# Kernel tuning notes

Measured on AMD Instinct MI355X. Metric: run time of the kernel, lower is better.

## Reference

```python
import jax, jax.numpy as jnp
import numpy as np

DIM = 512
HEADS = 8
RES = 14
HEAD_DIM = DIM // HEADS
N = RES * RES


def _make_bias_idxs(res):
    pts = [(i, j) for i in range(res) for j in range(res)]
    offs = {}
    idxs = []
    for p1 in pts:
        for p2 in pts:
            o = (abs(p1[0] - p2[0]), abs(p1[1] - p2[1]))
            if o not in offs:
                offs[o] = len(offs)
            idxs.append(offs[o])
    return np.asarray(idxs, dtype=np.int32).reshape(res * res, res * res), len(offs)


def setup_inputs() -> dict:
    key = jax.random.key(0)
    ks = jax.random.split(key, 6)
    idxs, n_off = _make_bias_idxs(RES)  # n_off == 196 for res=14
    B = 128
    return {
        "x": jax.random.normal(ks[0], (B, DIM, RES, RES), dtype=jnp.float32),
        "qkv_w": jax.random.normal(ks[1], (3 * DIM, DIM), dtype=jnp.float32) * 0.02,
        "qkv_b": jnp.zeros((3 * DIM,), dtype=jnp.float32),
        "proj_w": jax.random.normal(ks[2], (DIM, DIM), dtype=jnp.float32) * 0.02,
        "proj_b": jnp.zeros((DIM,), dtype=jnp.float32),
        "attention_biases": jax.random.normal(ks[3], (HEADS, n_off), dtype=jnp.float32) * 0.02,
        "bias_idxs": jnp.asarray(idxs),
    }


def reference(x, qkv_w, qkv_b, proj_w, proj_b, attention_biases, bias_idxs):
    B, C, H, W = x.shape
    scale = HEAD_DIM ** -0.5
    # 1x1 conv == channel-wise linear
    qkv = jnp.einsum("oc,bchw->bohw", qkv_w, x) + qkv_b[None, :, None, None]
    q, k, v = jnp.split(qkv, 3, axis=1)
    # [B, heads, head_dim, N]
    q = q.reshape(B, HEADS, HEAD_DIM, N)
    k = k.reshape(B, HEADS, HEAD_DIM, N)
    v = v.reshape(B, HEADS, HEAD_DIM, N)
    attn = jnp.einsum("bhdn,bhdm->bhnm", q, k) * scale  # [B,h,N,N]
    bias = attention_biases[:, bias_idxs]  # gather -> [h,N,N]
    attn = jax.nn.softmax(attn + bias[None], axis=-1)
    out = jnp.einsum("bhnm,bhdm->bhdn", attn, v).reshape(B, C, H, W)
    return jnp.einsum("oc,bchw->bohw", proj_w, out) + proj_b[None, :, None, None]
```

## Files before the change

### kernel.cpp

```cpp
#include <hip/hip_runtime.h>
#include <hip/hip_bf16.h>
#include <math.h>

#define B_     128
#define DIM_   512
#define HEADS_ 8
#define HD_    64
#define N_     196
#define NP_    224
#define NROW_  208
#define SCALE_ 0.125f
#define BSTRIDE (DIM_ * N_)
#define J_     (B_ * NP_)

typedef unsigned short u16;
typedef unsigned int   u32;
typedef __attribute__((ext_vector_type(8))) short bf16x8;
typedef __attribute__((ext_vector_type(4))) float f32x4;

__device__ __forceinline__ u16 f2bf(float f) {
    u32 u = __float_as_uint(f);
    return (u16)((u + 0x7fffu + ((u >> 16) & 1u)) >> 16);
}
__device__ __forceinline__ void gload_lds16(const u16* g, u16* l) {
    __builtin_amdgcn_global_load_lds(
        (const __attribute__((address_space(1))) void*)g,
        (__attribute__((address_space(3))) void*)l, 16, 0, 0);
}

__global__ __launch_bounds__(256) void cvt_bf(
    const float* __restrict__ src, u16* __restrict__ dst, int n4)
{
    const int i = blockIdx.x * 256 + threadIdx.x;
    if (i < n4) {
        const float4 v = reinterpret_cast<const float4*>(src)[i];
        uint2 o;
        o.x = (u32)f2bf(v.x) | ((u32)f2bf(v.y) << 16);
        o.y = (u32)f2bf(v.z) | ((u32)f2bf(v.w) << 16);
        reinterpret_cast<uint2*>(dst)[i] = o;
    }
}

__global__ __launch_bounds__(256) void cvt_xT(
    const float* __restrict__ x, u16* __restrict__ XT)
{
    __shared__ float tile[64][65];
    const int t = threadIdx.x;
    const int jj = t & 63, ii = t >> 6;
    const int ct = blockIdx.x, ntb = blockIdx.y, b = blockIdx.z;
    const float* xb = x + ((size_t)b * DIM_ + ct * 64) * N_;
    const int n0 = ntb * 64;
    #pragma unroll
    for (int s = 0; s < 16; ++s) {
        const int i = ii + s * 4;
        const int n = n0 + jj;
        tile[i][jj] = (n < N_) ? xb[(size_t)i * N_ + n] : 0.f;
    }
    __syncthreads();
    u16* ot = XT + (size_t)b * NP_ * DIM_ + ct * 64;
    #pragma unroll
    for (int s = 0; s < 16; ++s) {
        const int nn = n0 + ii + s * 4;
        if (nn < N_) ot[(size_t)nn * DIM_ + jj] = f2bf(tile[jj][ii + s * 4]);
    }
}

__global__ __launch_bounds__(256) void mk_eb(
    const float* __restrict__ biases, const int* __restrict__ bidx,
    float* __restrict__ EB)
{
    const int n = blockIdx.x, h = blockIdx.y;
    const int m = threadIdx.x;
    if (m < NP_) {
        float v = 0.f;
        if (n < N_ && m < N_) v = __expf(biases[h * N_ + bidx[n * N_ + m]]);
        EB[((size_t)h * NROW_ + n) * NP_ + m] = v;
    }
}

template<bool QKV>
__global__ __launch_bounds__(256) void gemm128(
    const u16* __restrict__ Bt, const u16* __restrict__ W,
    const float* __restrict__ bias,
    u16* __restrict__ o_q, u16* __restrict__ o_k, u16* __restrict__ o_v,
    float* __restrict__ o_f)
{
    __shared__ u16 As[128 * 32];
    __shared__ u16 Bs[128 * 32];
    const int t = threadIdx.x;
    const int wave = t >> 6, lane = t & 63;
    const int m16 = lane & 15, quad = lane >> 4;
    const int jt = blockIdx.x, mt = blockIdx.y;
    const int m0 = mt * 128, j0 = jt * 128;
    const int wy = wave >> 1, wx = wave & 1;

    const int srow  = (lane >> 2);
    const int schnk = (lane & 3) ^ ((lane >> 3) & 3);
    const u16* gA = W  + (size_t)(m0 + wave * 32 + srow) * DIM_ + schnk * 8;
    const u16* gB = Bt + (size_t)(j0 + wave * 32 + srow) * DIM_ + schnk * 8;

    const int rcol = (quad ^ ((m16 >> 1) & 3)) * 8;

    f32x4 acc[4][4];
    const f32x4 z4 = {0.f, 0.f, 0.f, 0.f};
    #pragma unroll
    for (int fi = 0; fi < 4; ++fi)
        #pragma unroll
        for (int fj = 0; fj < 4; ++fj) acc[fi][fj] = z4;

    for (int kt = 0; kt < 16; ++kt) {
        __syncthreads();
        #pragma unroll
        for (int cc = 0; cc < 2; ++cc) {
            const int c = wave * 2 + cc;
            gload_lds16(gA + (size_t)(cc * 16) * DIM_ + kt * 32, As + c * 512);
            gload_lds16(gB + (size_t)(cc * 16) * DIM_ + kt * 32, Bs + c * 512);
        }
        __syncthreads();
        bf16x8 af[4], bf[4];
        #pragma unroll
        for (int fi = 0; fi < 4; ++fi)
            af[fi] = *reinterpret_cast<const bf16x8*>(As + (wy * 64 + fi * 16 + m16) * 32 + rcol);
        #pragma unroll
        for (int fj = 0; fj < 4; ++fj)
            bf[fj] = *reinterpret_cast<const bf16x8*>(Bs + (wx * 64 + fj * 16 + m16) * 32 + rcol);
        #pragma unroll
        for (int fi = 0; fi < 4; ++fi)
            #pragma unroll
            for (int fj = 0; fj < 4; ++fj)
                acc[fi][fj] = __builtin_amdgcn_mfma_f32_16x16x32_bf16(af[fi], bf[fj], acc[fi][fj], 0, 0, 0);
    }

    const int mbase = m0 + wy * 64;
    float bb[4][4];
    #pragma unroll
    for (int fi = 0; fi < 4; ++fi)
        #pragma unroll
        for (int r = 0; r < 4; ++r) bb[fi][r] = bias[mbase + fi * 16 + quad * 4 + r];

    if (QKV) {
        const int part = mbase >> 9;
        const int h = (mbase & 511) >> 6;
        #pragma unroll
        for (int fj = 0; fj < 4; ++fj) {
            const int j = j0 + wx * 64 + fj * 16 + m16;
            const u32 b = (u32)j / 224u;
            const int n = j - (int)b * 224;
            if (part < 2) {
                u16* base = (part == 0 ? o_q : o_k) + (((size_t)b * HEADS_ + h) * NP_ + n) * HD_;
                #pragma unroll
                for (int fi = 0; fi < 4; ++fi) {
                    const int d0 = fi * 16 + quad * 4;
                    uint2 pk;
                    pk.x = (u32)f2bf(acc[fi][fj][0] + bb[fi][0]) | ((u32)f2bf(acc[fi][fj][1] + bb[fi][1]) << 16);
                    pk.y = (u32)f2bf(acc[fi][fj][2] + bb[fi][2]) | ((u32)f2bf(acc[fi][fj][3] + bb[fi][3]) << 16);
                    *reinterpret_cast<uint2*>(base + d0) = pk;
                }
            } else {
                u16* vb = o_v + (((size_t)b * HEADS_ + h) * HD_) * NP_ + n;
                #pragma unroll
                for (int fi = 0; fi < 4; ++fi) {
                    const int d0 = fi * 16 + quad * 4;
                    #pragma unroll
                    for (int r = 0; r < 4; ++r)
                        vb[(size_t)(d0 + r) * NP_] = f2bf(acc[fi][fj][r] + bb[fi][r]);
                }
            }
        }
    } else {
        #pragma unroll
        for (int fj = 0; fj < 4; ++fj) {
            const int j = j0 + wx * 64 + fj * 16 + m16;
            const u32 b = (u32)j / 224u;
            const int n = j - (int)b * 224;
            if (n < N_) {
                float* ob = o_f + (size_t)b * BSTRIDE + n;
                #pragma unroll
                for (int fi = 0; fi < 4; ++fi) {
                    const int r0 = mbase + fi * 16 + quad * 4;
                    #pragma unroll
                    for (int r = 0; r < 4; ++r)
                        ob[(size_t)(r0 + r) * N_] = acc[fi][fj][r] + bb[fi][r];
                }
            }
        }
    }
}

__global__ __launch_bounds__(512) void attn_mfma(
    const u16* __restrict__ qT, const u16* __restrict__ kT,
    const u16* __restrict__ vS, const float* __restrict__ EB,
    u16* __restrict__ OT)
{
    __shared__ u16 Ks[224 * 64];
    __shared__ u16 Vs[64 * 232];
    __shared__ u16 P[8][16 * 232];
    const int t = threadIdx.x;
    const int wave = t >> 6, lane = t & 63;
    const int m16 = lane & 15, quad = lane >> 4;
    const int b = blockIdx.x, h = blockIdx.y;
    const u16* qTb = qT + ((size_t)b * HEADS_ + h) * (NP_ * HD_);
    const u16* kTb = kT + ((size_t)b * HEADS_ + h) * (NP_ * HD_);
    const u16* vb  = vS + ((size_t)b * HEADS_ + h) * (HD_ * NP_);
    const float* ebh = EB + (size_t)h * NROW_ * NP_;
    u16* Pw = P[wave];
    u16* otb = OT + (size_t)b * NP_ * DIM_ + h * HD_;
    const f32x4 z4 = {0.f, 0.f, 0.f, 0.f};

    #pragma unroll
    for (int i = 0; i < 4; ++i) {
        const int c = t + i * 512;
        if (c < 1792) {
            const int row = c >> 3, ch = c & 7;
            const bf16x8 d = *reinterpret_cast<const bf16x8*>(kTb + row * HD_ + ch * 8);
            *reinterpret_cast<bf16x8*>(Ks + row * 64 + ((ch ^ (row & 7)) * 8)) = d;
        }
    }
    #pragma unroll
    for (int i = 0; i < 4; ++i) {
        const int c = t + i * 512;
        if (c < 1792) {
            const u32 row = (u32)c / 28u;
            const int ch = c - (int)row * 28;
            const bf16x8 d = *reinterpret_cast<const bf16x8*>(vb + (size_t)row * NP_ + ch * 8);
            *reinterpret_cast<bf16x8*>(Vs + row * 232 + ch * 8) = d;
        }
    }
    __syncthreads();

    for (int nt = wave; nt < 13; nt += 8) {
        f32x4 s[14];
        #pragma unroll
        for (int mt = 0; mt < 14; ++mt) s[mt] = z4;
        #pragma unroll
        for (int ks = 0; ks < 2; ++ks) {
            const bf16x8 a = *reinterpret_cast<const bf16x8*>(
                qTb + (size_t)(nt * 16 + m16) * HD_ + ks * 32 + quad * 8);
            const int ch = ((ks * 4 + quad) ^ (m16 & 7)) * 8;
            #pragma unroll
            for (int mtile = 0; mtile < 14; ++mtile) {
                const bf16x8 bf = *reinterpret_cast<const bf16x8*>(
                    Ks + (mtile * 16 + m16) * 64 + ch);
                s[mtile] = __builtin_amdgcn_mfma_f32_16x16x32_bf16(a, bf, s[mtile], 0, 0, 0);
            }
        }
        float mx[4] = {-INFINITY, -INFINITY, -INFINITY, -INFINITY};
        #pragma unroll
        for (int mt = 0; mt < 14; ++mt)
            #pragma unroll
            for (int r = 0; r < 4; ++r) mx[r] = fmaxf(mx[r], s[mt][r]);
        #pragma unroll
        for (int off = 1; off < 16; off <<= 1)
            #pragma unroll
            for (int r = 0; r < 4; ++r) mx[r] = fmaxf(mx[r], __shfl_xor(mx[r], off, 64));
        #pragma unroll
        for (int r = 0; r < 4; ++r) mx[r] *= SCALE_;

        const float* ebn = ebh + (size_t)(nt * 16 + quad * 4) * NP_ + m16;
        float sum[4] = {0.f, 0.f, 0.f, 0.f};
        #pragma unroll
        for (int mt = 0; mt < 14; ++mt) {
            #pragma unroll
            for (int r = 0; r < 4; ++r) {
                const float e = __expf(fmaf(s[mt][r], SCALE_, -mx[r])) * ebn[(size_t)r * NP_ + mt * 16];
                s[mt][r] = e;
                sum[r] += e;
            }
        }
        #pragma unroll
        for (int off = 1; off < 16; off <<= 1)
            #pragma unroll
            for (int r = 0; r < 4; ++r) sum[r] += __shfl_xor(sum[r], off, 64);
        float inv[4];
        #pragma unroll
        for (int r = 0; r < 4; ++r) inv[r] = 1.f / sum[r];

        #pragma unroll
        for (int mt = 0; mt < 14; ++mt)
            #pragma unroll
            for (int r = 0; r < 4; ++r)
                Pw[(quad * 4 + r) * 232 + mt * 16 + m16] = f2bf(s[mt][r] * inv[r]);

        f32x4 o[4];
        #pragma unroll
        for (int dt = 0; dt < 4; ++dt) o[dt] = z4;
        #pragma unroll
        for (int ks = 0; ks < 7; ++ks) {
            const bf16x8 a = *reinterpret_cast<const bf16x8*>(Pw + m16 * 232 + ks * 32 + quad * 8);
            #pragma unroll
            for (int dt = 0; dt < 4; ++dt) {
                const bf16x8 bf = *reinterpret_cast<const bf16x8*>(
                    Vs + (dt * 16 + m16) * 232 + ks * 32 + quad * 8);
                o[dt] = __builtin_amdgcn_mfma_f32_16x16x32_bf16(a, bf, o[dt], 0, 0, 0);
            }
        }
        #pragma unroll
        for (int r = 0; r < 4; ++r) {
            const int n = nt * 16 + quad * 4 + r;
            if (n < N_) {
                #pragma unroll
                for (int dt = 0; dt < 4; ++dt)
                    otb[(size_t)n * DIM_ + dt * 16 + m16] = f2bf(o[dt][r]);
            }
        }
    }
}

extern "C" void kernel_launch(void* const* d_in, const int* in_sizes, int n_in,
                              void* d_out, int out_size, void* d_ws, size_t ws_size,
                              hipStream_t stream) {
    const float* x      = (const float*)d_in[0];
    const float* qkv_w  = (const float*)d_in[1];
    const float* qkv_b  = (const float*)d_in[2];
    const float* proj_w = (const float*)d_in[3];
    const float* proj_b = (const float*)d_in[4];
    const float* biases = (const float*)d_in[5];
    const int*   bidx   = (const int*)d_in[6];
    float* out = (float*)d_out;

    char* w = (char*)d_ws;
    u16* XT  = (u16*)w; w += (size_t)B_ * NP_ * DIM_ * 2;
    u16* qTw = (u16*)w; w += (size_t)B_ * HEADS_ * NP_ * HD_ * 2;
    u16* vSw = (u16*)w; w += (size_t)B_ * HEADS_ * HD_ * NP_ * 2;
    float* EB = (float*)w; w += (size_t)HEADS_ * NROW_ * NP_ * 4;
    u16* wq  = (u16*)w; w += (size_t)3 * DIM_ * DIM_ * 2;
    u16* wpj = (u16*)w;
    u16* kTw = (u16*)d_out;

    cvt_bf<<<(3 * DIM_ * DIM_ / 4 + 255) / 256, 256, 0, stream>>>(qkv_w, wq, 3 * DIM_ * DIM_ / 4);
    cvt_bf<<<(DIM_ * DIM_ / 4 + 255) / 256, 256, 0, stream>>>(proj_w, wpj, DIM_ * DIM_ / 4);
    cvt_xT<<<dim3(8, 4, B_), 256, 0, stream>>>(x, XT);
    mk_eb<<<dim3(NROW_, HEADS_), 256, 0, stream>>>(biases, bidx, EB);
    gemm128<true><<<dim3(J_ / 128, 12), 256, 0, stream>>>(XT, wq, qkv_b, qTw, kTw, vSw, nullptr);
    attn_mfma<<<dim3(B_, HEADS_), 512, 0, stream>>>(qTw, kTw, vSw, EB, XT);
    gemm128<false><<<dim3(J_ / 128, 4), 256, 0, stream>>>(XT, wpj, proj_b, nullptr, nullptr, nullptr, out);
}
```

Before: 290.4 us.

## Double-buffer GEMM LDS tiles, swizzle workgroup order, merge weight conversions

The two 128x128 bf16 MFMA GEMMs now use two LDS buffers: the next K-slice is loaded asynchronously while the current one is consumed. This removes one barrier per K step and hides global-load latency. The grid is flattened to 1D and blocks are remapped with an 8-way swizzle that groups tiles sharing W/X rows, meant to improve cache locality across XCDs. The two weight-conversion launches are merged into one 2D launch. LDS use doubles, which may lower occupancy.

```diff
diff --git a/kernel.cpp b/kernel.cpp
--- a/kernel.cpp
+++ b/kernel.cpp
@@ -28,10 +28,14 @@
         (__attribute__((address_space(3))) void*)l, 16, 0, 0);
 }
 
-__global__ __launch_bounds__(256) void cvt_bf(
-    const float* __restrict__ src, u16* __restrict__ dst, int n4)
+__global__ __launch_bounds__(256) void cvt_bf2(
+    const float* __restrict__ a, u16* __restrict__ da, int n4a,
+    const float* __restrict__ b, u16* __restrict__ db, int n4b)
 {
     const int i = blockIdx.x * 256 + threadIdx.x;
+    const float* src = blockIdx.y ? b : a;
+    u16* dst = blockIdx.y ? db : da;
+    const int n4 = blockIdx.y ? n4b : n4a;
     if (i < n4) {
         const float4 v = reinterpret_cast<const float4*>(src)[i];
         uint2 o;
@@ -85,12 +89,18 @@
     u16* __restrict__ o_q, u16* __restrict__ o_k, u16* __restrict__ o_v,
     float* __restrict__ o_f)
 {
-    __shared__ u16 As[128 * 32];
-    __shared__ u16 Bs[128 * 32];
+    __shared__ u16 As[2][128 * 32];
+    __shared__ u16 Bs[2][128 * 32];
     const int t = threadIdx.x;
     const int wave = t >> 6, lane = t & 63;
     const int m16 = lane & 15, quad = lane >> 4;
-    const int jt = blockIdx.x, mt = blockIdx.y;
+
+    constexpr int MT  = QKV ? 12 : 4;
+    constexpr int NWG = (J_ / 128) * MT;
+    const int bid = blockIdx.x;
+    const int swz = (bid & 7) * (NWG / 8) + (bid >> 3);
+    const int mt = swz % MT;
+    const int jt = swz / MT;
     const int m0 = mt * 128, j0 = jt * 128;
     const int wy = wave >> 1, wx = wave & 1;
 
@@ -108,22 +118,31 @@
         #pragma unroll
         for (int fj = 0; fj < 4; ++fj) acc[fi][fj] = z4;
 
+    #pragma unroll
+    for (int cc = 0; cc < 2; ++cc) {
+        const int c = wave * 2 + cc;
+        gload_lds16(gA + (size_t)(cc * 16) * DIM_, As[0] + c * 512);
+        gload_lds16(gB + (size_t)(cc * 16) * DIM_, Bs[0] + c * 512);
+    }
+    #pragma unroll
     for (int kt = 0; kt < 16; ++kt) {
+        const int cur = kt & 1;
         __syncthreads();
-        #pragma unroll
-        for (int cc = 0; cc < 2; ++cc) {
-            const int c = wave * 2 + cc;
-            gload_lds16(gA + (size_t)(cc * 16) * DIM_ + kt * 32, As + c * 512);
-            gload_lds16(gB + (size_t)(cc * 16) * DIM_ + kt * 32, Bs + c * 512);
-        }
-        __syncthreads();
+        if (kt < 15) {
+            #pragma unroll
+            for (int cc = 0; cc < 2; ++cc) {
+                const int c = wave * 2 + cc;
+                gload_lds16(gA + (size_t)(cc * 16) * DIM_ + (kt + 1) * 32, As[cur ^ 1] + c * 512);
+                gload_lds16(gB + (size_t)(cc * 16) * DIM_ + (kt + 1) * 32, Bs[cur ^ 1] + c * 512);
+            }
+        }
         bf16x8 af[4], bf[4];
         #pragma unroll
         for (int fi = 0; fi < 4; ++fi)
-            af[fi] = *reinterpret_cast<const bf16x8*>(As + (wy * 64 + fi * 16 + m16) * 32 + rcol);
+            af[fi] = *reinterpret_cast<const bf16x8*>(As[cur] + (wy * 64 + fi * 16 + m16) * 32 + rcol);
         #pragma unroll
         for (int fj = 0; fj < 4; ++fj)
-            bf[fj] = *reinterpret_cast<const bf16x8*>(Bs + (wx * 64 + fj * 16 + m16) * 32 + rcol);
+            bf[fj] = *reinterpret_cast<const bf16x8*>(Bs[cur] + (wx * 64 + fj * 16 + m16) * 32 + rcol);
         #pragma unroll
         for (int fi = 0; fi < 4; ++fi)
             #pragma unroll
@@ -327,11 +346,11 @@
     u16* wpj = (u16*)w;
     u16* kTw = (u16*)d_out;
 
-    cvt_bf<<<(3 * DIM_ * DIM_ / 4 + 255) / 256, 256, 0, stream>>>(qkv_w, wq, 3 * DIM_ * DIM_ / 4);
-    cvt_bf<<<(DIM_ * DIM_ / 4 + 255) / 256, 256, 0, stream>>>(proj_w, wpj, DIM_ * DIM_ / 4);
+    cvt_bf2<<<dim3(768, 2), 256, 0, stream>>>(qkv_w, wq, 3 * DIM_ * DIM_ / 4,
+                                              proj_w, wpj, DIM_ * DIM_ / 4);
     cvt_xT<<<dim3(8, 4, B_), 256, 0, stream>>>(x, XT);
     mk_eb<<<dim3(NROW_, HEADS_), 256, 0, stream>>>(biases, bidx, EB);
-    gemm128<true><<<dim3(J_ / 128, 12), 256, 0, stream>>>(XT, wq, qkv_b, qTw, kTw, vSw, nullptr);
+    gemm128<true><<<dim3((J_ / 128) * 12), 256, 0, stream>>>(XT, wq, qkv_b, qTw, kTw, vSw, nullptr);
     attn_mfma<<<dim3(B_, HEADS_), 512, 0, stream>>>(qTw, kTw, vSw, EB, XT);
-    gemm128<false><<<dim3(J_ / 128, 4), 256, 0, stream>>>(XT, wpj, proj_b, nullptr, nullptr, nullptr, out);
-}
+    gemm128<false><<<dim3((J_ / 128) * 4), 256, 0, stream>>>(XT, wpj, proj_b, nullptr, nullptr, nullptr, out);
+}
```

Result: faster. 276.5 us (-4.8%).
